# Kernel optimization log

Measured on AMD Instinct MI355X. Metric: run time of the kernel, lower is better.

## Reference

```python
import jax, jax.numpy as jnp
import numpy as np
from jax import lax

# Model dims (match init_kwargs config)
HID = 2048      # hidden_size
NH = 64         # num_heads
P = 64          # head_dim
N = 128         # ssm_state_size
G = 1           # n_groups
CS = 256        # chunk_size
K = 4           # conv kernel
D_INNER = NH * P                  # 4096
CONV_DIM = D_INNER + 2 * G * N    # 4352
PROJ = D_INNER + CONV_DIM + NH    # 8512
EPS = 1e-5
BATCH, SEQ = 2, 2048


def setup_inputs() -> dict:
    key = jax.random.key(0)
    ks = jax.random.split(key, 8)
    hidden_states = jax.random.normal(ks[0], (BATCH, SEQ, HID), dtype=jnp.float32)
    W_in = jax.random.normal(ks[1], (PROJ, HID), dtype=jnp.float32) * 0.02
    conv_w = jax.random.normal(ks[2], (CONV_DIM, 1, K), dtype=jnp.float32) * 0.2
    conv_b = jax.random.normal(ks[3], (CONV_DIM,), dtype=jnp.float32) * 0.02
    # dt_bias initialized like inv-softplus of dt in [1e-3, 1e-1]
    dt = jnp.exp(jax.random.uniform(ks[4], (NH,)) * (np.log(0.1) - np.log(0.001)) + np.log(0.001))
    dt_bias = (dt + jnp.log(-jnp.expm1(-dt))).astype(jnp.float32)
    A_log = jnp.log(jnp.arange(1, NH + 1, dtype=jnp.float32))
    D_param = jnp.ones((NH,), dtype=jnp.float32)
    norm_w = jnp.ones((D_INNER,), dtype=jnp.float32)
    W_out = jax.random.normal(ks[5], (HID, D_INNER), dtype=jnp.float32) * 0.02
    return {"hidden_states": hidden_states, "W_in": W_in, "conv_w": conv_w,
            "conv_b": conv_b, "dt_bias": dt_bias, "A_log": A_log,
            "D_param": D_param, "norm_w": norm_w, "W_out": W_out}


def _segsum(x):
    # x: (..., c) -> (..., c, c); seg[i, j] = sum_{j < k <= i} x_k (diag 0), -inf above diag
    T = x.shape[-1]
    xc = jnp.cumsum(x, axis=-1)
    seg = xc[..., :, None] - xc[..., None, :]
    mask = jnp.tril(jnp.ones((T, T), dtype=bool))
    return jnp.where(mask, seg, -jnp.inf)


def _mamba2_forward(hidden_states, W_in, conv_w, conv_b, dt_bias, A_log, D_param, norm_w, W_out):
    B_, L_ = hidden_states.shape[:2]
    proj = hidden_states @ W_in.T                           # (b, l, PROJ)
    z = proj[..., :D_INNER]                                 # gate
    xBC = proj[..., D_INNER:D_INNER + CONV_DIM]
    dt = proj[..., D_INNER + CONV_DIM:]                     # (b, l, NH)

    # depthwise causal conv1d + silu
    xc = lax.conv_general_dilated(
        jnp.transpose(xBC, (0, 2, 1)), conv_w,
        window_strides=(1,), padding=[(K - 1, 0)],
        feature_group_count=CONV_DIM)                        # (b, CONV_DIM, l)
    xc = xc + conv_b[None, :, None]
    xBC = jax.nn.silu(jnp.transpose(xc, (0, 2, 1)))          # (b, l, CONV_DIM)

    x = xBC[..., :D_INNER].reshape(B_, L_, NH, P)
    Bm = xBC[..., D_INNER:D_INNER + G * N].reshape(B_, L_, G, N)
    Cm = xBC[..., D_INNER + G * N:].reshape(B_, L_, G, N)

    dt = jax.nn.softplus(dt + dt_bias)                       # (b, l, NH)
    A = -jnp.exp(A_log)                                      # (NH,)

    Bh = jnp.repeat(Bm, NH // G, axis=2)                     # (b, l, h, n)
    Ch = jnp.repeat(Cm, NH // G, axis=2)

    # ---- chunked SSD scan ----
    nc = L_ // CS
    x_dt = (x * dt[..., None]).reshape(B_, nc, CS, NH, P)    # (b, c, s, h, p)
    B_c = Bh.reshape(B_, nc, CS, NH, N)
    C_c = Ch.reshape(B_, nc, CS, NH, N)
    dA = jnp.transpose((dt * A).reshape(B_, nc, CS, NH), (0, 3, 1, 2))  # (b, h, c, s)
    A_cum = jnp.cumsum(dA, axis=-1)                          # (b, h, c, s)

    Lmat = jnp.exp(_segsum(dA))                              # (b, h, c, s, s)
    Y_diag = jnp.einsum('bclhn,bcshn,bhcls,bcshp->bclhp', C_c, B_c, Lmat, x_dt)

    decay_states = jnp.exp(A_cum[..., -1:] - A_cum)          # (b, h, c, s)
    states = jnp.einsum('bclhn,bhcl,bclhp->bchpn', B_c, decay_states, x_dt)

    da_last = A_cum[..., -1]                                 # (b, h, c)

    def step(prev, inp):
        s_k, d_k = inp                                       # (b,h,p,n), (b,h)
        new = prev * jnp.exp(d_k)[..., None, None] + s_k
        return new, prev

    _, prev_states = lax.scan(step, jnp.zeros((B_, NH, P, N), dtype=x.dtype),
                              (jnp.transpose(states, (1, 0, 2, 3, 4)),
                               jnp.transpose(da_last, (2, 0, 1))))
    prev_states = jnp.transpose(prev_states, (1, 2, 0, 3, 4))  # (b, h, c, p, n)

    Y_off = jnp.einsum('bclhn,bhcpn,bhcl->bclhp', C_c, prev_states, jnp.exp(A_cum))

    y = (Y_diag + Y_off).reshape(B_, L_, NH, P) + D_param[None, None, :, None] * x
    y = y.reshape(B_, L_, D_INNER)

    # gated grouped RMSNorm (norm_before_gate=False): norm(y * silu(z)) * w
    g = y * jax.nn.silu(z)
    gs = D_INNER // G
    gr = g.reshape(B_, L_, G, gs)
    var = jnp.mean(gr * gr, axis=-1, keepdims=True)
    gn = (gr * lax.rsqrt(var + EPS)).reshape(B_, L_, D_INNER) * norm_w

    return gn @ W_out.T                                      # (b, l, HID)


def reference(hidden_states, W_in, conv_w, conv_b, dt_bias, A_log, D_param, norm_w, W_out):
    return _mamba2_forward(hidden_states, W_in, conv_w, conv_b, dt_bias, A_log, D_param, norm_w, W_out)
```

## Files before the change

### kernel.cpp

```cpp
#include <hip/hip_runtime.h>

#define SEQLEN 2048
#define NHEADS 64
#define PDIM 64
#define NSTATE 128
#define CSIZE 256
#define NCHUNK 8
#define DINNER 4096
#define CONVD 4352
#define PROJD 8512

using s8v = __attribute__((ext_vector_type(8))) short;
using f4v = __attribute__((ext_vector_type(4))) float;
using bf8v = __attribute__((ext_vector_type(8))) __bf16;

__device__ __forceinline__ short f2bf(float x) {
  union { float f; unsigned u; } t; t.f = x;
  unsigned r = t.u + 0x7FFFu + ((t.u >> 16) & 1u);
  return (short)(r >> 16);
}
__device__ __forceinline__ float bf2f(short s) {
  union { unsigned u; float f; } t;
  t.u = ((unsigned)(unsigned short)s) << 16;
  return t.f;
}

__device__ __forceinline__ f4v mfma_bf16(s8v a, s8v b, f4v c) {
  return __builtin_amdgcn_mfma_f32_16x16x32_bf16(
      __builtin_bit_cast(bf8v, a), __builtin_bit_cast(bf8v, b), c, 0, 0, 0);
}

__device__ __forceinline__ void gll16(const void* g, void* l) {
  __builtin_amdgcn_global_load_lds(
      (const __attribute__((address_space(1))) unsigned*)g,
      (__attribute__((address_space(3))) unsigned*)l, 16, 0, 0);
}

__global__ __launch_bounds__(256) void cast_bf16_kernel(
    const float* __restrict__ in, short* __restrict__ out, int n4) {
  int i = blockIdx.x * 256 + threadIdx.x;
  if (i < n4) {
    float4 v = ((const float4*)in)[i];
    short4 o;
    o.x = f2bf(v.x); o.y = f2bf(v.y); o.z = f2bf(v.z); o.w = f2bf(v.w);
    ((short4*)out)[i] = o;
  }
}

__global__ __launch_bounds__(256, 4) void gemm1_kernel(
    const short* __restrict__ A, const short* __restrict__ B,
    short* __restrict__ z, short* __restrict__ xbc, float* __restrict__ dtb) {
  const int K = 2048;
  const int bid = blockIdx.x;
  const int panel = bid / (67 * 4), rem = bid % (67 * 4);
  const int bx = rem >> 2, by = panel * 4 + (rem & 3);
  const int tn0 = bx * 128, tm0 = by * 128;
  __shared__ alignas(16) short lds[8704];
  short* As = lds;
  short* Bs = lds + 4096;
  short* Cs = lds;
  const int tid = threadIdx.x;
  const int lane = tid & 63, wid = tid >> 6;
  const int wm = (wid >> 1) * 64, wn = (wid & 1) * 64;
  const int lr = lane & 15, q = lane >> 4;
  const int fA = (lr & 3) ^ ((lr >> 2) & 3);
  const int qs = (q ^ fA) * 8;
  f4v acc[4][4];
  for (int i = 0; i < 4; i++)
    for (int j = 0; j < 4; j++)
      for (int r = 0; r < 4; r++) acc[i][j][r] = 0.f;

  for (int k0 = 0; k0 < K; k0 += 32) {
    __syncthreads();
    for (int it = 0; it < 2; it++) {
      int ci = it * 256 + tid;
      int row = ci >> 2;
      int cg = ((ci & 3) ^ (row & 3) ^ ((row >> 2) & 3)) << 3;
      gll16(&A[(size_t)(tm0 + row) * K + k0 + cg], &As[ci * 8]);
      gll16(&B[(size_t)(tn0 + row) * K + k0 + cg], &Bs[ci * 8]);
    }
    __syncthreads();
    s8v af[4], bfr[4];
    for (int i = 0; i < 4; i++) af[i]  = *(const s8v*)&As[(wm + i * 16 + lr) * 32 + qs];
    for (int j = 0; j < 4; j++) bfr[j] = *(const s8v*)&Bs[(wn + j * 16 + lr) * 32 + qs];
    for (int i = 0; i < 4; i++)
      for (int j = 0; j < 4; j++)
        acc[i][j] = mfma_bf16(af[i], bfr[j], acc[i][j]);
  }
  __syncthreads();

  if (tn0 < 8448) {
    short* outp; int rowstride, colbase;
    if (tn0 < DINNER) { outp = z;   rowstride = DINNER; colbase = tn0; }
    else              { outp = xbc; rowstride = CONVD;  colbase = tn0 - DINNER; }
    for (int hh = 0; hh < 2; hh++) {
      if ((wid >> 1) == hh) {
        for (int i = 0; i < 4; i++)
          for (int j = 0; j < 4; j++)
            for (int r = 0; r < 4; r++)
              Cs[(i * 16 + q * 4 + r) * 136 + wn + j * 16 + lr] = f2bf(acc[i][j][r]);
      }
      __syncthreads();
      for (int ps = 0; ps < 4; ps++) {
        int idx = ps * 256 + tid;
        int r = idx >> 4, c8 = (idx & 15) * 8;
        s8v v = *(const s8v*)&Cs[r * 136 + c8];
        *(s8v*)&outp[(size_t)(tm0 + hh * 64 + r) * rowstride + colbase + c8] = v;
      }
      __syncthreads();
    }
  } else {
    for (int i = 0; i < 4; i++)
      for (int j = 0; j < 4; j++) {
        int c0 = tn0 + wn + j * 16 + lr;
        if (c0 < PROJD)
          for (int r = 0; r < 4; r++)
            dtb[(size_t)(tm0 + wm + i * 16 + q * 4 + r) * NHEADS + (c0 - 8448)] =
                acc[i][j][r];
      }
  }
}

__global__ __launch_bounds__(256, 4) void gemm_nt_bf16(
    const short* __restrict__ A, const short* __restrict__ B,
    float* __restrict__ C, int M, int N, int K) {
  const int nbx = N >> 7;
  const int bid = blockIdx.x;
  const int panel = bid / (nbx * 4), rem = bid % (nbx * 4);
  const int bx = rem >> 2, by = panel * 4 + (rem & 3);
  const int tn0 = bx * 128, tm0 = by * 128;
  __shared__ alignas(16) short As[128 * 32];
  __shared__ alignas(16) short Bs[128 * 32];
  const int tid = threadIdx.x;
  const int lane = tid & 63, wid = tid >> 6;
  const int wm = (wid >> 1) * 64, wn = (wid & 1) * 64;
  const int lr = lane & 15, q = lane >> 4;
  const int fA = (lr & 3) ^ ((lr >> 2) & 3);
  const int qs = (q ^ fA) * 8;
  f4v acc[4][4];
  for (int i = 0; i < 4; i++)
    for (int j = 0; j < 4; j++)
      for (int r = 0; r < 4; r++) acc[i][j][r] = 0.f;

  for (int k0 = 0; k0 < K; k0 += 32) {
    __syncthreads();
    for (int it = 0; it < 2; it++) {
      int ci = it * 256 + tid;
      int row = ci >> 2;
      int cg = ((ci & 3) ^ (row & 3) ^ ((row >> 2) & 3)) << 3;
      gll16(&A[(size_t)(tm0 + row) * K + k0 + cg], &As[ci * 8]);
      gll16(&B[(size_t)(tn0 + row) * K + k0 + cg], &Bs[ci * 8]);
    }
    __syncthreads();
    s8v af[4], bfr[4];
    for (int i = 0; i < 4; i++) af[i]  = *(const s8v*)&As[(wm + i * 16 + lr) * 32 + qs];
    for (int j = 0; j < 4; j++) bfr[j] = *(const s8v*)&Bs[(wn + j * 16 + lr) * 32 + qs];
    for (int i = 0; i < 4; i++)
      for (int j = 0; j < 4; j++)
        acc[i][j] = mfma_bf16(af[i], bfr[j], acc[i][j]);
  }
  for (int i = 0; i < 4; i++)
    for (int j = 0; j < 4; j++) {
      int r0 = tm0 + wm + i * 16 + q * 4;
      int c0 = tn0 + wn + j * 16 + lr;
      for (int r = 0; r < 4; r++)
        C[(size_t)(r0 + r) * N + c0] = acc[i][j][r];
    }
}

__global__ __launch_bounds__(256) void conv_silu_kernel(
    const short* __restrict__ xbc, const float* __restrict__ conv_w,
    const float* __restrict__ conv_b, short* __restrict__ xBCc) {
  int cc = blockIdx.x * 256 + threadIdx.x;
  int bl = blockIdx.y;
  int b = bl >> 11, l = bl & 2047;
  float4 wv = *(const float4*)&conv_w[cc * 4];
  float wk[4] = {wv.x, wv.y, wv.z, wv.w};
  float acc = conv_b[cc];
  const short* pbase = xbc + (size_t)(b * SEQLEN) * CONVD + cc;
#pragma unroll
  for (int k = 0; k < 4; k++) {
    int ls = l - 3 + k;
    if (ls >= 0) acc += bf2f(pbase[(size_t)ls * CONVD]) * wk[k];
  }
  float sv = acc / (1.f + expf(-acc));
  xBCc[(size_t)bl * CONVD + cc] = f2bf(sv);
}

__global__ __launch_bounds__(256) void dt_kernel(
    float* __restrict__ dtb, const float* __restrict__ dt_bias) {
  int idx = blockIdx.x * 256 + threadIdx.x;
  int hh = idx & 63;
  float v = dtb[idx] + dt_bias[hh];
  dtb[idx] = (v > 20.f) ? v : log1pf(expf(v));
}

__global__ __launch_bounds__(256) void ssd_states_kernel(
    const short* __restrict__ xBCc, const float* __restrict__ dtp,
    const float* __restrict__ A_log, short* __restrict__ states,
    float* __restrict__ da_last) {
  const int blk = blockIdx.x;
  const int h = blk & 63, cc = (blk >> 6) & 7, b = blk >> 9;
  const int tid = threadIdx.x;
  __shared__ float dt_s[CSIZE], Acum[CSIZE], w_s[CSIZE];
  __shared__ float xw[64][64];
  __shared__ float Bt[64][NSTATE];
  const size_t row0 = (size_t)(b * SEQLEN + cc * CSIZE);
  dt_s[tid] = dtp[(row0 + tid) * NHEADS + h];
  __syncthreads();
  if (tid == 0) {
    float Aval = -expf(A_log[h]);
    float s = 0.f;
    for (int i = 0; i < CSIZE; i++) { s += dt_s[i]; Acum[i] = s * Aval; }
    da_last[(size_t)(b * NHEADS + h) * NCHUNK + cc] = Acum[CSIZE - 1];
  }
  __syncthreads();
  float total = Acum[CSIZE - 1];
  w_s[tid] = dt_s[tid] * expf(total - Acum[tid]);
  float acc[4][8];
  for (int a = 0; a < 4; a++) for (int j = 0; j < 8; j++) acc[a][j] = 0.f;
  const int pi = (tid & 15) * 4, ni = (tid >> 4) * 8;
  for (int lt = 0; lt < 4; lt++) {
    __syncthreads();
    for (int i = 0; i < 4; i++) {
      int idx = tid + i * 256;
      int r = idx >> 4, c4 = (idx & 15) << 2;
      short4 v = *(const short4*)&xBCc[(row0 + lt * 64 + r) * CONVD + h * PDIM + c4];
      float wl = w_s[lt * 64 + r];
      xw[r][c4 + 0] = bf2f(v.x) * wl;
      xw[r][c4 + 1] = bf2f(v.y) * wl;
      xw[r][c4 + 2] = bf2f(v.z) * wl;
      xw[r][c4 + 3] = bf2f(v.w) * wl;
    }
    for (int i = 0; i < 8; i++) {
      int idx = tid + i * 256;
      int r = idx >> 5, c4 = (idx & 31) << 2;
      short4 v = *(const short4*)&xBCc[(row0 + lt * 64 + r) * CONVD + DINNER + c4];
      Bt[r][c4 + 0] = bf2f(v.x);
      Bt[r][c4 + 1] = bf2f(v.y);
      Bt[r][c4 + 2] = bf2f(v.z);
      Bt[r][c4 + 3] = bf2f(v.w);
    }
    __syncthreads();
    for (int l = 0; l < 64; l++) {
      float4 xv = *(const float4*)&xw[l][pi];
      float4 b0 = *(const float4*)&Bt[l][ni];
      float4 b1 = *(const float4*)&Bt[l][ni + 4];
      float xa[4] = {xv.x, xv.y, xv.z, xv.w};
      float bb[8] = {b0.x, b0.y, b0.z, b0.w, b1.x, b1.y, b1.z, b1.w};
      for (int a = 0; a < 4; a++)
        for (int j = 0; j < 8; j++)
          acc[a][j] += xa[a] * bb[j];
    }
  }
  const size_t sbase = (((size_t)b * NCHUNK + cc) * NHEADS + h) * (PDIM * NSTATE);
  for (int a = 0; a < 4; a++) {
    short o[8];
    for (int j = 0; j < 8; j++) o[j] = f2bf(acc[a][j]);
    *(s8v*)&states[sbase + (size_t)(pi + a) * NSTATE + ni] = *(const s8v*)o;
  }
}

__global__ __launch_bounds__(256) void scan_kernel(
    short* __restrict__ states, const float* __restrict__ da_last) {
  const int bh = blockIdx.x >> 2, sl = blockIdx.x & 3;
  const int b = bh >> 6, h = bh & 63;
  const int tid = threadIdx.x;
  float prev[8];
  for (int i = 0; i < 8; i++) prev[i] = 0.f;
  for (int c = 0; c < NCHUNK; c++) {
    const size_t base = (((size_t)b * NCHUNK + c) * NHEADS + h) * (PDIM * NSTATE)
                      + sl * 2048;
    const float d = expf(da_last[(size_t)bh * NCHUNK + c]);
    for (int i = 0; i < 8; i++) {
      size_t e = base + tid + i * 256;
      float s = bf2f(states[e]);
      states[e] = f2bf(prev[i]);
      prev[i] = prev[i] * d + s;
    }
  }
}

__global__ __launch_bounds__(256) void ssd_y_kernel(
    const short* __restrict__ xBCc, const float* __restrict__ dtp,
    const float* __restrict__ A_log, const float* __restrict__ D_param,
    const short* __restrict__ prevs, short* __restrict__ y) {
  const int blk = blockIdx.x;
  const int h = blk & 63, cc = (blk >> 6) & 7, b = blk >> 9;
  const int tid = threadIdx.x;
  const int lane = tid & 63, w = tid >> 6;
  const int lr = lane & 15, q = lane >> 4;
  __shared__ float dt_s[CSIZE];
  __shared__ float Acum[CSIZE];
  __shared__ short C_s[64][136];
  __shared__ short BP_s[64][136];
  __shared__ short xdtT[64][72];
  __shared__ short Mt[64][72];
  const size_t row0 = (size_t)(b * SEQLEN + cc * CSIZE);
  dt_s[tid] = dtp[(row0 + tid) * NHEADS + h];
  __syncthreads();
  if (tid == 0) {
    float Aval = -expf(A_log[h]);
    float s = 0.f;
    for (int i = 0; i < CSIZE; i++) { s += dt_s[i]; Acum[i] = s * Aval; }
  }
  const float Dh = D_param[h];
  const size_t prevbase = (((size_t)b * NCHUNK + cc) * NHEADS + h) * (PDIM * NSTATE);
  const int wl0 = w * 16;

  for (int lt = 0; lt < 4; lt++) {
    __syncthreads();
    for (int i = 0; i < 4; i++) {
      int idx = tid + i * 256;
      int r = idx >> 4, c8 = (idx & 15) << 3;
      *(s8v*)&C_s[r][c8] =
          *(const s8v*)&xBCc[(row0 + lt * 64 + r) * CONVD + DINNER + NSTATE + c8];
      *(s8v*)&BP_s[r][c8] = *(const s8v*)&prevs[prevbase + (size_t)r * NSTATE + c8];
    }
    __syncthreads();
    f4v acc[4];
    for (int j = 0; j < 4; j++) for (int r = 0; r < 4; r++) acc[j][r] = 0.f;
    for (int ks = 0; ks < 4; ks++) {
      s8v a = *(const s8v*)&C_s[wl0 + lr][ks * 32 + q * 8];
      for (int j = 0; j < 4; j++) {
        s8v bb = *(const s8v*)&BP_s[j * 16 + lr][ks * 32 + q * 8];
        acc[j] = mfma_bf16(a, bb, acc[j]);
      }
    }
    for (int r = 0; r < 4; r++) {
      float e = __expf(Acum[lt * 64 + wl0 + q * 4 + r]);
      for (int j = 0; j < 4; j++) acc[j][r] *= e;
    }
    for (int st = 0; st <= lt; st++) {
      __syncthreads();
      for (int i = 0; i < 4; i++) {
        int idx = tid + i * 256;
        int r = idx >> 4, c8 = (idx & 15) << 3;
        *(s8v*)&BP_s[r][c8] =
            *(const s8v*)&xBCc[(row0 + st * 64 + r) * CONVD + DINNER + c8];
      }
      for (int i = 0; i < 4; i++) {
        int idx = tid + i * 256;
        int r = idx >> 4, c4 = (idx & 15) << 2;
        float dtv = dt_s[st * 64 + r];
        short4 v = *(const short4*)&xBCc[(row0 + st * 64 + r) * CONVD + h * PDIM + c4];
        xdtT[c4 + 0][r] = f2bf(bf2f(v.x) * dtv);
        xdtT[c4 + 1][r] = f2bf(bf2f(v.y) * dtv);
        xdtT[c4 + 2][r] = f2bf(bf2f(v.z) * dtv);
        xdtT[c4 + 3][r] = f2bf(bf2f(v.w) * dtv);
      }
      __syncthreads();
      f4v sacc[4];
      for (int j = 0; j < 4; j++) for (int r = 0; r < 4; r++) sacc[j][r] = 0.f;
      for (int ks = 0; ks < 4; ks++) {
        s8v a = *(const s8v*)&C_s[wl0 + lr][ks * 32 + q * 8];
        for (int j = 0; j < 4; j++) {
          s8v bb = *(const s8v*)&BP_s[j * 16 + lr][ks * 32 + q * 8];
          sacc[j] = mfma_bf16(a, bb, sacc[j]);
        }
      }
      int lbase = lt * 64 + wl0 + q * 4;
      for (int j = 0; j < 4; j++) {
        int sg = st * 64 + j * 16 + lr;
        for (int r = 0; r < 4; r++) {
          int ll = lbase + r;
          float m = (sg <= ll) ? sacc[j][r] * __expf(Acum[ll] - Acum[sg]) : 0.f;
          Mt[wl0 + q * 4 + r][j * 16 + lr] = f2bf(m);
        }
      }
      __syncthreads();
      for (int ss2 = 0; ss2 < 2; ss2++) {
        s8v a = *(const s8v*)&Mt[wl0 + lr][ss2 * 32 + q * 8];
        for (int j = 0; j < 4; j++) {
          s8v bb = *(const s8v*)&xdtT[j * 16 + lr][ss2 * 32 + q * 8];
          acc[j] = mfma_bf16(a, bb, acc[j]);
        }
      }
    }
    for (int j = 0; j < 4; j++)
      for (int r = 0; r < 4; r++) {
        int lrow = wl0 + q * 4 + r;
        int ll = lt * 64 + lrow;
        int p = j * 16 + lr;
        float xv = bf2f(xBCc[(row0 + ll) * CONVD + h * PDIM + p]);
        Mt[lrow][p] = f2bf(acc[j][r] + Dh * xv);
      }
    __syncthreads();
    for (int ps = 0; ps < 2; ps++) {
      int r = ps * 32 + (tid >> 3);
      int c8 = (tid & 7) * 8;
      s8v v = *(const s8v*)&Mt[r][c8];
      *(s8v*)&y[(row0 + lt * 64 + r) * DINNER + h * PDIM + c8] = v;
    }
  }
}

__global__ __launch_bounds__(256) void norm_kernel(
    const short* __restrict__ y, const short* __restrict__ z,
    const float* __restrict__ norm_w, short* __restrict__ g) {
  int bl = blockIdx.x, tid = threadIdx.x;
  const short4* yrow = (const short4*)(y + (size_t)bl * DINNER);
  const short4* zrow = (const short4*)(z + (size_t)bl * DINNER);
  float gv[16];
  float ss = 0.f;
  for (int i = 0; i < 4; i++) {
    short4 yv = yrow[tid + i * 256];
    short4 zv = zrow[tid + i * 256];
    float zf[4] = {bf2f(zv.x), bf2f(zv.y), bf2f(zv.z), bf2f(zv.w)};
    float yf[4] = {bf2f(yv.x), bf2f(yv.y), bf2f(yv.z), bf2f(yv.w)};
    for (int t = 0; t < 4; t++) {
      float gg = yf[t] * (zf[t] / (1.f + expf(-zf[t])));
      gv[i * 4 + t] = gg;
      ss += gg * gg;
    }
  }
  for (int off = 32; off > 0; off >>= 1) ss += __shfl_down(ss, off);
  __shared__ float red[4];
  __shared__ float rsS;
  if ((tid & 63) == 0) red[tid >> 6] = ss;
  __syncthreads();
  if (tid == 0) rsS = rsqrtf((red[0] + red[1] + red[2] + red[3]) * (1.f / 4096.f) + 1e-5f);
  __syncthreads();
  float rs = rsS;
  for (int i = 0; i < 4; i++) {
    int j4 = (tid + i * 256) * 4;
    float4 nw = *(const float4*)&norm_w[j4];
    short4 o;
    o.x = f2bf(gv[i * 4 + 0] * rs * nw.x);
    o.y = f2bf(gv[i * 4 + 1] * rs * nw.y);
    o.z = f2bf(gv[i * 4 + 2] * rs * nw.z);
    o.w = f2bf(gv[i * 4 + 3] * rs * nw.w);
    *(short4*)&g[(size_t)bl * DINNER + j4] = o;
  }
}

extern "C" void kernel_launch(void* const* d_in, const int* in_sizes, int n_in,
                              void* d_out, int out_size, void* d_ws, size_t ws_size,
                              hipStream_t stream) {
  const float* hidden  = (const float*)d_in[0];
  const float* W_in    = (const float*)d_in[1];
  const float* conv_w  = (const float*)d_in[2];
  const float* conv_b  = (const float*)d_in[3];
  const float* dt_bias = (const float*)d_in[4];
  const float* A_log   = (const float*)d_in[5];
  const float* D_param = (const float*)d_in[6];
  const float* norm_w  = (const float*)d_in[7];
  const float* W_out   = (const float*)d_in[8];
  float* out = (float*)d_out;

  char* ws = (char*)d_ws;
  short* z_bf  = (short*)(ws + 0);
  float* dtb   = (float*)(ws + 33554432);
  float* da_l  = (float*)(ws + 34603008);
  short* xbc_pre = (short*)(ws + 34607104);
  short* y_bf    = (short*)(ws + 34607104);
  short* hid_bf  = (short*)(ws + 70258688);
  short* win_bf  = (short*)(ws + 87035904);
  short* xBCc    = (short*)(ws + 70258688);
  short* states  = (short*)(ws + 105910272);
  short* g_bf    = (short*)(ws + 70258688);
  short* wout_bf = (short*)(ws + 105910272);
  if (ws_size < (size_t)122687488) return;

  cast_bf16_kernel<<<8192, 256, 0, stream>>>(hidden, hid_bf, 2097152);
  cast_bf16_kernel<<<17024, 256, 0, stream>>>(W_in, win_bf, 4358144);

  gemm1_kernel<<<2144, 256, 0, stream>>>(hid_bf, win_bf, z_bf, xbc_pre, dtb);

  conv_silu_kernel<<<dim3(17, 4096), 256, 0, stream>>>(xbc_pre, conv_w, conv_b, xBCc);
  dt_kernel<<<1024, 256, 0, stream>>>(dtb, dt_bias);

  ssd_states_kernel<<<1024, 256, 0, stream>>>(xBCc, dtb, A_log, states, da_l);
  scan_kernel<<<512, 256, 0, stream>>>(states, da_l);
  ssd_y_kernel<<<1024, 256, 0, stream>>>(xBCc, dtb, A_log, D_param, states, y_bf);

  norm_kernel<<<4096, 256, 0, stream>>>(y_bf, z_bf, norm_w, g_bf);
  cast_bf16_kernel<<<8192, 256, 0, stream>>>(W_out, wout_bf, 2097152);

  gemm_nt_bf16<<<512, 256, 0, stream>>>(g_bf, wout_bf, out, 4096, 2048, 4096);
}
```

Baseline: 698.0 us.

## Preload whole-chunk B and scaled-x tiles in ssd_y_kernel, use per-wave scratch

ssd_y_kernel now loads the chunk's full B matrix (256x128), the dt-scaled transposed x (64x256) and the previous-state tile into shared memory once, instead of reloading them inside the lt/st loops. The M matrix and the output staging go into a per-wave buffer, which removes most block-wide __syncthreads in the inner loop. The aim is to cut redundant global loads and barrier stalls. In exchange, LDS use rises to roughly 140KB and launch_bounds(256,1) is set, which limits occupancy to about one block per CU.

```diff
diff --git a/kernel.cpp b/kernel.cpp
--- a/kernel.cpp
+++ b/kernel.cpp
@@ -281,7 +281,7 @@
   }
 }
 
-__global__ __launch_bounds__(256) void ssd_y_kernel(
+__global__ __launch_bounds__(256, 1) void ssd_y_kernel(
     const short* __restrict__ xBCc, const float* __restrict__ dtp,
     const float* __restrict__ A_log, const float* __restrict__ D_param,
     const short* __restrict__ prevs, short* __restrict__ y) {
@@ -290,40 +290,81 @@
   const int tid = threadIdx.x;
   const int lane = tid & 63, w = tid >> 6;
   const int lr = lane & 15, q = lane >> 4;
+
   __shared__ float dt_s[CSIZE];
   __shared__ float Acum[CSIZE];
-  __shared__ short C_s[64][136];
-  __shared__ short BP_s[64][136];
-  __shared__ short xdtT[64][72];
-  __shared__ short Mt[64][72];
+  __shared__ alignas(16) short B_s[256 * 136];
+  __shared__ alignas(16) short xdtT[64 * 264];
+  __shared__ alignas(16) short prev_s[64 * 136];
+  __shared__ alignas(16) short C_s[64 * 136];
+  __shared__ alignas(16) short Mt[4][16 * 72];
+
   const size_t row0 = (size_t)(b * SEQLEN + cc * CSIZE);
   dt_s[tid] = dtp[(row0 + tid) * NHEADS + h];
   __syncthreads();
+
+  short* tmp = B_s;
+  for (int i = 0; i < 8; i++) {
+    int idx = tid + i * 256;
+    int r = idx >> 3, c8 = (idx & 7) * 8;
+    *(s8v*)&tmp[r * 72 + c8] =
+        *(const s8v*)&xBCc[(row0 + r) * CONVD + h * PDIM + c8];
+  }
   if (tid == 0) {
     float Aval = -expf(A_log[h]);
     float s = 0.f;
     for (int i = 0; i < CSIZE; i++) { s += dt_s[i]; Acum[i] = s * Aval; }
   }
+  __syncthreads();
+
+  {
+    int p = tid & 63, sblk = tid >> 6;
+    for (int j = 0; j < 8; j++) {
+      short pack[8];
+#pragma unroll
+      for (int k = 0; k < 8; k++) {
+        int s = sblk * 64 + j * 8 + k;
+        pack[k] = f2bf(bf2f(tmp[s * 72 + p]) * dt_s[s]);
+      }
+      *(s8v*)&xdtT[p * 264 + sblk * 64 + j * 8] = *(const s8v*)pack;
+    }
+  }
+  __syncthreads();
+
+  for (int i = 0; i < 16; i++) {
+    int idx = tid + i * 256;
+    int r = idx >> 4, c8 = (idx & 15) * 8;
+    *(s8v*)&B_s[r * 136 + c8] =
+        *(const s8v*)&xBCc[(row0 + r) * CONVD + DINNER + c8];
+  }
+  const size_t prevbase = (((size_t)b * NCHUNK + cc) * NHEADS + h) * (PDIM * NSTATE);
+  for (int i = 0; i < 4; i++) {
+    int idx = tid + i * 256;
+    int r = idx >> 4, c8 = (idx & 15) * 8;
+    *(s8v*)&prev_s[r * 136 + c8] = *(const s8v*)&prevs[prevbase + (size_t)r * NSTATE + c8];
+  }
+  __syncthreads();
+
   const float Dh = D_param[h];
-  const size_t prevbase = (((size_t)b * NCHUNK + cc) * NHEADS + h) * (PDIM * NSTATE);
   const int wl0 = w * 16;
+  short* mt = &Mt[w][0];
 
   for (int lt = 0; lt < 4; lt++) {
     __syncthreads();
     for (int i = 0; i < 4; i++) {
       int idx = tid + i * 256;
-      int r = idx >> 4, c8 = (idx & 15) << 3;
-      *(s8v*)&C_s[r][c8] =
+      int r = idx >> 4, c8 = (idx & 15) * 8;
+      *(s8v*)&C_s[r * 136 + c8] =
           *(const s8v*)&xBCc[(row0 + lt * 64 + r) * CONVD + DINNER + NSTATE + c8];
-      *(s8v*)&BP_s[r][c8] = *(const s8v*)&prevs[prevbase + (size_t)r * NSTATE + c8];
-    }
-    __syncthreads();
+    }
+    __syncthreads();
+
     f4v acc[4];
     for (int j = 0; j < 4; j++) for (int r = 0; r < 4; r++) acc[j][r] = 0.f;
     for (int ks = 0; ks < 4; ks++) {
-      s8v a = *(const s8v*)&C_s[wl0 + lr][ks * 32 + q * 8];
+      s8v a = *(const s8v*)&C_s[(wl0 + lr) * 136 + ks * 32 + q * 8];
       for (int j = 0; j < 4; j++) {
-        s8v bb = *(const s8v*)&BP_s[j * 16 + lr][ks * 32 + q * 8];
+        s8v bb = *(const s8v*)&prev_s[(j * 16 + lr) * 136 + ks * 32 + q * 8];
         acc[j] = mfma_bf16(a, bb, acc[j]);
       }
     }
@@ -331,31 +372,14 @@
       float e = __expf(Acum[lt * 64 + wl0 + q * 4 + r]);
       for (int j = 0; j < 4; j++) acc[j][r] *= e;
     }
+
     for (int st = 0; st <= lt; st++) {
-      __syncthreads();
-      for (int i = 0; i < 4; i++) {
-        int idx = tid + i * 256;
-        int r = idx >> 4, c8 = (idx & 15) << 3;
-        *(s8v*)&BP_s[r][c8] =
-            *(const s8v*)&xBCc[(row0 + st * 64 + r) * CONVD + DINNER + c8];
-      }
-      for (int i = 0; i < 4; i++) {
-        int idx = tid + i * 256;
-        int r = idx >> 4, c4 = (idx & 15) << 2;
-        float dtv = dt_s[st * 64 + r];
-        short4 v = *(const short4*)&xBCc[(row0 + st * 64 + r) * CONVD + h * PDIM + c4];
-        xdtT[c4 + 0][r] = f2bf(bf2f(v.x) * dtv);
-        xdtT[c4 + 1][r] = f2bf(bf2f(v.y) * dtv);
-        xdtT[c4 + 2][r] = f2bf(bf2f(v.z) * dtv);
-        xdtT[c4 + 3][r] = f2bf(bf2f(v.w) * dtv);
-      }
-      __syncthreads();
       f4v sacc[4];
       for (int j = 0; j < 4; j++) for (int r = 0; r < 4; r++) sacc[j][r] = 0.f;
       for (int ks = 0; ks < 4; ks++) {
-        s8v a = *(const s8v*)&C_s[wl0 + lr][ks * 32 + q * 8];
+        s8v a = *(const s8v*)&C_s[(wl0 + lr) * 136 + ks * 32 + q * 8];
         for (int j = 0; j < 4; j++) {
-          s8v bb = *(const s8v*)&BP_s[j * 16 + lr][ks * 32 + q * 8];
+          s8v bb = *(const s8v*)&B_s[(st * 64 + j * 16 + lr) * 136 + ks * 32 + q * 8];
           sacc[j] = mfma_bf16(a, bb, sacc[j]);
         }
       }
@@ -365,32 +389,32 @@
         for (int r = 0; r < 4; r++) {
           int ll = lbase + r;
           float m = (sg <= ll) ? sacc[j][r] * __expf(Acum[ll] - Acum[sg]) : 0.f;
-          Mt[wl0 + q * 4 + r][j * 16 + lr] = f2bf(m);
+          mt[(q * 4 + r) * 72 + j * 16 + lr] = f2bf(m);
         }
       }
-      __syncthreads();
       for (int ss2 = 0; ss2 < 2; ss2++) {
-        s8v a = *(const s8v*)&Mt[wl0 + lr][ss2 * 32 + q * 8];
+        s8v a = *(const s8v*)&mt[lr * 72 + ss2 * 32 + q * 8];
         for (int j = 0; j < 4; j++) {
-          s8v bb = *(const s8v*)&xdtT[j * 16 + lr][ss2 * 32 + q * 8];
+          s8v bb = *(const s8v*)&xdtT[(j * 16 + lr) * 264 + st * 64 + ss2 * 32 + q * 8];
           acc[j] = mfma_bf16(a, bb, acc[j]);
         }
       }
     }
+
     for (int j = 0; j < 4; j++)
       for (int r = 0; r < 4; r++) {
-        int lrow = wl0 + q * 4 + r;
-        int ll = lt * 64 + lrow;
+        int ll = lt * 64 + wl0 + q * 4 + r;
         int p = j * 16 + lr;
         float xv = bf2f(xBCc[(row0 + ll) * CONVD + h * PDIM + p]);
-        Mt[lrow][p] = f2bf(acc[j][r] + Dh * xv);
-      }
-    __syncthreads();
-    for (int ps = 0; ps < 2; ps++) {
-      int r = ps * 32 + (tid >> 3);
-      int c8 = (tid & 7) * 8;
-      s8v v = *(const s8v*)&Mt[r][c8];
-      *(s8v*)&y[(row0 + lt * 64 + r) * DINNER + h * PDIM + c8] = v;
+        mt[(q * 4 + r) * 72 + p] = f2bf(acc[j][r] + Dh * xv);
+      }
+    {
+      int r = lane >> 2, c8 = (lane & 3) * 8;
+      s8v v0 = *(const s8v*)&mt[r * 72 + c8];
+      s8v v1 = *(const s8v*)&mt[r * 72 + c8 + 32];
+      size_t yb = (row0 + lt * 64 + wl0 + r) * DINNER + h * PDIM;
+      *(s8v*)&y[yb + c8] = v0;
+      *(s8v*)&y[yb + c8 + 32] = v1;
     }
   }
 }
```

New measurement: 715.8 us. 1.03x slower.
